# Kernel optimization log

Hardware: AMD Instinct MI355X
Metric: run time of the kernel (lower is better)

## Reference

```python
import jax, jax.numpy as jnp
import numpy as np

ALPHA = 4.0   # spikingjelly surrogate.Sigmoid default
TAU = 2.0
VTH = 1.0
EPS = 1e-5

@jax.custom_vjp
def spike(x):
    return (x >= 0.0).astype(x.dtype)

def _spike_fwd(x):
    return spike(x), x

def _spike_bwd(x, g):
    s = jax.nn.sigmoid(ALPHA * x)
    return (g * ALPHA * s * (1.0 - s),)

spike.defvjp(_spike_fwd, _spike_bwd)

def lif(x):
    # x: [T, B, N, C]; multi-step LIF, v_reset=0 hard reset, detach_reset=True
    def step(v, xt):
        v = v + (xt - v) / TAU          # charge
        s = spike(v - VTH)              # fire (surrogate grad)
        v = v * (1.0 - jax.lax.stop_gradient(s))  # hard reset, detached
        return v, s
    _, out = jax.lax.scan(step, jnp.zeros_like(x[0]), x)
    return out

def bn(x, gamma, beta):
    # BatchNorm1d in training mode: per-channel (last dim) over all other dims
    mu = x.mean(axis=(0, 1, 2), keepdims=True)
    var = x.var(axis=(0, 1, 2), keepdims=True)  # biased var, as torch BN uses for normalization
    return (x - mu) * jax.lax.rsqrt(var + EPS) * gamma + beta

def setup_inputs() -> dict:
    key = jax.random.key(0)
    ks = jax.random.split(key, 3)
    T, B, N, C, H = 4, 32, 1024, 256, 256
    x = jax.random.normal(ks[0], (T, B, N, C), dtype=jnp.float32)
    W1 = jax.random.normal(ks[1], (C, H), dtype=jnp.float32) * (1.0 / np.sqrt(C))
    W2 = jax.random.normal(ks[2], (H, C), dtype=jnp.float32) * (1.0 / np.sqrt(H))
    return {
        "x": x,
        "W1": W1, "b1": jnp.zeros((H,), jnp.float32),
        "gamma1": jnp.ones((H,), jnp.float32), "beta1": jnp.zeros((H,), jnp.float32),
        "W2": W2, "b2": jnp.zeros((C,), jnp.float32),
        "gamma2": jnp.ones((C,), jnp.float32), "beta2": jnp.zeros((C,), jnp.float32),
    }

def reference(x, W1, b1, gamma1, beta1, W2, b2, gamma2, beta2):
    # fc1: Linear -> BN (per-channel over T*B*N) -> multi-step LIF
    h = jnp.einsum('tbnc,ch->tbnh', x, W1) + b1
    h = lif(bn(h, gamma1, beta1))
    # fc2
    o = jnp.einsum('tbnh,ho->tbno', h, W2) + b2
    return lif(bn(o, gamma2, beta2))
```

## Files before the change

kernel.cpp:

```cpp
#include <hip/hip_runtime.h>


typedef __attribute__((ext_vector_type(8))) short bf16x8;
typedef __attribute__((ext_vector_type(8))) _Float16 f16x8;
typedef __attribute__((ext_vector_type(4))) _Float16 f16x4;
typedef __attribute__((ext_vector_type(4))) float f32x4;

__device__ __forceinline__ unsigned short f32_to_bf16_rne(float f) {
    unsigned int u = __builtin_bit_cast(unsigned int, f);
    u += 0x7FFFu + ((u >> 16) & 1u);
    return (unsigned short)(u >> 16);
}
__device__ __forceinline__ float bf16_to_f32(unsigned short h) {
    unsigned int u = ((unsigned int)h) << 16;
    return __builtin_bit_cast(float, u);
}

__global__ __launch_bounds__(256) void split_w1(const float* __restrict__ W1,
                                                _Float16* __restrict__ BhiT,
                                                _Float16* __restrict__ BloT) {
    int i = blockIdx.x * 256 + threadIdx.x;
    int k = i >> 8, n = i & 255;
    float w = W1[i];
    _Float16 hi = (_Float16)w;
    _Float16 lo = (_Float16)((w - (float)hi) * 4096.0f);
    BhiT[(size_t)n * 256 + k] = hi;
    BloT[(size_t)n * 256 + k] = lo;
}

__global__ __launch_bounds__(256) void split_w2(const float* __restrict__ W2,
                                                unsigned short* __restrict__ Bt) {
    int i = blockIdx.x * 256 + threadIdx.x;
    int k = i >> 8, n = i & 255;
    float w = W2[i];
    unsigned short hi = f32_to_bf16_rne(w);
    float r = w - bf16_to_f32(hi);
    unsigned short mid = f32_to_bf16_rne(r);
    float r2 = r - bf16_to_f32(mid);
    unsigned short lo = f32_to_bf16_rne(r2);
    Bt[(size_t)(0 * 256 + n) * 256 + k] = hi;
    Bt[(size_t)(1 * 256 + n) * 256 + k] = mid;
    Bt[(size_t)(2 * 256 + n) * 256 + k] = lo;
}

__global__ __launch_bounds__(512) void gemm1_mfma(const float* __restrict__ A,
                                                  const _Float16* __restrict__ Bhi,
                                                  const _Float16* __restrict__ Blo,
                                                  const float* __restrict__ bias,
                                                  float* __restrict__ C,
                                                  double* __restrict__ partial) {
    __shared__ __align__(16) _Float16 Ahi[128 * 256];
    __shared__ __align__(16) _Float16 Alo[128 * 256];
    const size_t m0 = (size_t)blockIdx.x * 128;
    const int tid = threadIdx.x;
    const int lane = tid & 63;
    const int wave = tid >> 6;
    const int wr = wave >> 2;
    const int wc = wave & 3;
    const int lrow = lane & 15, lchunk = lane >> 4;

    const _Float16* BhiB = Bhi + ((size_t)(64 * wc + lrow)) * 256 + lchunk * 8;
    const _Float16* BloB = Blo + ((size_t)(64 * wc + lrow)) * 256 + lchunk * 8;

    f16x8 bh[2][4], bl[2][4];
#define LOADB1(buf, kk)                                                   \
    _Pragma("unroll") for (int nf = 0; nf < 4; ++nf) {                    \
        bh[buf][nf] = *(const f16x8*)(BhiB + nf * 4096 + (kk) * 32);      \
        bl[buf][nf] = *(const f16x8*)(BloB + nf * 4096 + (kk) * 32);      \
    }

    LOADB1(0, 0)

    {
        const float* src = A + m0 * 256;
#pragma unroll
        for (int it = 0; it < 16; ++it) {
            unsigned i4 = (unsigned)(it * 512 + tid);
            float4 v = *(const float4*)(src + (size_t)i4 * 4);
            float f[4] = {v.x, v.y, v.z, v.w};
            f16x4 hi4, lo4;
#pragma unroll
            for (int e = 0; e < 4; ++e) {
                _Float16 hh = (_Float16)f[e];
                hi4[e] = hh;
                lo4[e] = (_Float16)((f[e] - (float)hh) * 4096.0f);
            }
            unsigned off = i4 * 8u;
            unsigned swz = off ^ (((off >> 9) & 7u) << 4);
            *(f16x4*)((char*)Ahi + swz) = hi4;
            *(f16x4*)((char*)Alo + swz) = lo4;
        }
    }
    __syncthreads();

    f32x4 acc0[4][4] = {}, acc1[4][4] = {};

#pragma unroll
    for (int k0 = 0; k0 < 8; ++k0) {
        const int cur = k0 & 1;
        if (k0 < 7) { LOADB1(cur ^ 1, k0 + 1) }
        f16x8 ah[4], al[4];
#pragma unroll
        for (int mf = 0; mf < 4; ++mf) {
            unsigned r = (unsigned)(64 * wr + 16 * mf + lrow);
            unsigned off = (r * 512u + (unsigned)(k0 * 64 + lchunk * 16)) ^ ((r & 7u) << 4);
            ah[mf] = *(const f16x8*)((const char*)Ahi + off);
            al[mf] = *(const f16x8*)((const char*)Alo + off);
        }
#pragma unroll
        for (int nf = 0; nf < 4; ++nf)
#pragma unroll
            for (int mf = 0; mf < 4; ++mf)
                acc0[mf][nf] = __builtin_amdgcn_mfma_f32_16x16x32_f16(
                    ah[mf], bh[cur][nf], acc0[mf][nf], 0, 0, 0);
#pragma unroll
        for (int nf = 0; nf < 4; ++nf)
#pragma unroll
            for (int mf = 0; mf < 4; ++mf)
                acc1[mf][nf] = __builtin_amdgcn_mfma_f32_16x16x32_f16(
                    ah[mf], bl[cur][nf], acc1[mf][nf], 0, 0, 0);
#pragma unroll
        for (int nf = 0; nf < 4; ++nf)
#pragma unroll
            for (int mf = 0; mf < 4; ++mf)
                acc1[mf][nf] = __builtin_amdgcn_mfma_f32_16x16x32_f16(
                    al[mf], bh[cur][nf], acc1[mf][nf], 0, 0, 0);
    }
#undef LOADB1

    const float UNSCALE = 1.0f / 4096.0f;
    double s[4], q[4];
#pragma unroll
    for (int nf = 0; nf < 4; ++nf) {
        int col = 64 * wc + 16 * nf + lrow;
        float bvv = bias[col];
        double ss = 0.0, qq = 0.0;
#pragma unroll
        for (int mf = 0; mf < 4; ++mf) {
            size_t rowb = m0 + 64 * wr + 16 * mf + 4 * lchunk;
#pragma unroll
            for (int e = 0; e < 4; ++e) {
                float hv = acc0[mf][nf][e] + acc1[mf][nf][e] * UNSCALE + bvv;
                C[(rowb + e) * 256 + col] = hv;
                ss += (double)hv;
                qq += (double)hv * (double)hv;
            }
        }
        s[nf] = ss;
        q[nf] = qq;
    }
#pragma unroll
    for (int nf = 0; nf < 4; ++nf) {
        s[nf] += __shfl_xor(s[nf], 16);
        s[nf] += __shfl_xor(s[nf], 32);
        q[nf] += __shfl_xor(q[nf], 16);
        q[nf] += __shfl_xor(q[nf], 32);
    }
    __syncthreads();
    double* shred = (double*)Ahi;
    if (lane < 16) {
#pragma unroll
        for (int nf = 0; nf < 4; ++nf) {
            shred[(wave * 4 + nf) * 16 + lane] = s[nf];
            shred[512 + (wave * 4 + nf) * 16 + lane] = q[nf];
        }
    }
    __syncthreads();
    if (wave < 4) {
        int nf = lane >> 4, lr = lane & 15;
        int col = 64 * wave + 16 * nf + lr;
        double ssum = shred[(wave * 4 + nf) * 16 + lr] +
                      shred[((4 + wave) * 4 + nf) * 16 + lr];
        double qsum = shred[512 + (wave * 4 + nf) * 16 + lr] +
                      shred[512 + ((4 + wave) * 4 + nf) * 16 + lr];
        partial[(size_t)blockIdx.x * 512 + col] = ssum;
        partial[(size_t)blockIdx.x * 512 + 256 + col] = qsum;
    }
}

__global__ __launch_bounds__(512) void gemm2_fused(const float* __restrict__ h,
                                                   const float2* __restrict__ ss1,
                                                   const unsigned short* __restrict__ Bt,
                                                   const float* __restrict__ bias,
                                                   float* __restrict__ C,
                                                   double* __restrict__ partial,
                                                   int bnRows) {
    __shared__ __align__(16) unsigned short Asw[128 * 256];
    const int bn0 = blockIdx.x * 32;
    const int tid = threadIdx.x;
    const int lane = tid & 63;
    const int wave = tid >> 6;
    const int wr = wave >> 2;
    const int wc = wave & 3;
    const int lrow = lane & 15, lchunk = lane >> 4;

    const unsigned short* Bbase =
        Bt + ((size_t)(64 * wc + lrow)) * 256 + lchunk * 8;

    bf16x8 bb[2][12];
#define LOADB(buf, kk)                                                        \
    _Pragma("unroll") for (int t = 0; t < 3; ++t)                             \
    _Pragma("unroll") for (int nf = 0; nf < 4; ++nf)                          \
        bb[buf][t * 4 + nf] = *(const bf16x8*)(Bbase + (size_t)t * 65536 +    \
                                               nf * 4096 + (kk) * 32);

    LOADB(0, 0)

    {
#pragma unroll
        for (int it = 0; it < 4; ++it) {
            int slot = it * 512 + tid;
            int bn = slot >> 6;
            int colq = slot & 63;
            int c0 = colq * 4;
            float2 p0 = ss1[c0], p1 = ss1[c0 + 1], p2 = ss1[c0 + 2], p3 = ss1[c0 + 3];
            float4 v = make_float4(0.f, 0.f, 0.f, 0.f);
#pragma unroll
            for (int t = 0; t < 4; ++t) {
                float4 hv = *(const float4*)(h + ((size_t)t * bnRows + bn0 + bn) * 256 + c0);
                float x0 = hv.x * p0.x + p0.y;
                float x1 = hv.y * p1.x + p1.y;
                float x2 = hv.z * p2.x + p2.y;
                float x3 = hv.w * p3.x + p3.y;
                v.x = (v.x + x0) * 0.5f;
                v.y = (v.y + x1) * 0.5f;
                v.z = (v.z + x2) * 0.5f;
                v.w = (v.w + x3) * 0.5f;
                ushort4 sp;
                sp.x = (v.x >= 1.0f) ? 0x3F80 : 0;
                sp.y = (v.y >= 1.0f) ? 0x3F80 : 0;
                sp.z = (v.z >= 1.0f) ? 0x3F80 : 0;
                sp.w = (v.w >= 1.0f) ? 0x3F80 : 0;
                v.x = (v.x >= 1.0f) ? 0.0f : v.x;
                v.y = (v.y >= 1.0f) ? 0.0f : v.y;
                v.z = (v.z >= 1.0f) ? 0.0f : v.z;
                v.w = (v.w >= 1.0f) ? 0.0f : v.w;
                unsigned row = (unsigned)(t * 32 + bn);
                unsigned off = (row * 512u + (unsigned)colq * 8u) ^ ((row & 7u) << 4);
                *(ushort4*)((char*)Asw + off) = sp;
            }
        }
    }
    __syncthreads();

    f32x4 acc[4][4] = {};

#pragma unroll
    for (int k0 = 0; k0 < 8; ++k0) {
        const int cur = k0 & 1;
        if (k0 < 7) { LOADB(cur ^ 1, k0 + 1) }
        bf16x8 af[4];
#pragma unroll
        for (int mf = 0; mf < 4; ++mf) {
            unsigned r = (unsigned)(64 * wr + 16 * mf + lrow);
            unsigned off = r * 512u + (unsigned)(k0 * 64 + lchunk * 16);
            off ^= ((r & 7u) << 4);
            af[mf] = *(const bf16x8*)((const char*)Asw + off);
        }
#pragma unroll
        for (int t = 0; t < 3; ++t)
#pragma unroll
            for (int nf = 0; nf < 4; ++nf)
#pragma unroll
                for (int mf = 0; mf < 4; ++mf)
                    acc[mf][nf] = __builtin_amdgcn_mfma_f32_16x16x32_bf16(
                        af[mf], bb[cur][t * 4 + nf], acc[mf][nf], 0, 0, 0);
    }
#undef LOADB

    double s[4], q[4];
#pragma unroll
    for (int nf = 0; nf < 4; ++nf) {
        int col = 64 * wc + 16 * nf + lrow;
        float bvv = bias[col];
        double ss = 0.0, qq = 0.0;
#pragma unroll
        for (int mf = 0; mf < 4; ++mf) {
            int Lbase = 64 * wr + 16 * mf + 4 * lchunk;
#pragma unroll
            for (int e = 0; e < 4; ++e) {
                int L = Lbase + e;
                size_t G = (size_t)(L >> 5) * bnRows + bn0 + (L & 31);
                float hv = acc[mf][nf][e] + bvv;
                C[G * 256 + col] = hv;
                ss += (double)hv;
                qq += (double)hv * (double)hv;
            }
        }
        s[nf] = ss;
        q[nf] = qq;
    }
#pragma unroll
    for (int nf = 0; nf < 4; ++nf) {
        s[nf] += __shfl_xor(s[nf], 16);
        s[nf] += __shfl_xor(s[nf], 32);
        q[nf] += __shfl_xor(q[nf], 16);
        q[nf] += __shfl_xor(q[nf], 32);
    }
    __syncthreads();
    double* shred = (double*)Asw;
    if (lane < 16) {
#pragma unroll
        for (int nf = 0; nf < 4; ++nf) {
            shred[(wave * 4 + nf) * 16 + lane] = s[nf];
            shred[512 + (wave * 4 + nf) * 16 + lane] = q[nf];
        }
    }
    __syncthreads();
    if (wave < 4) {
        int nf = lane >> 4, lr = lane & 15;
        int col = 64 * wave + 16 * nf + lr;
        double ssum = shred[(wave * 4 + nf) * 16 + lr] +
                      shred[((4 + wave) * 4 + nf) * 16 + lr];
        double qsum = shred[512 + (wave * 4 + nf) * 16 + lr] +
                      shred[512 + ((4 + wave) * 4 + nf) * 16 + lr];
        partial[(size_t)blockIdx.x * 512 + col] = ssum;
        partial[(size_t)blockIdx.x * 512 + 256 + col] = qsum;
    }
}

__global__ __launch_bounds__(256) void finalize_stats(const double* __restrict__ partial,
                                                      const float* __restrict__ gamma,
                                                      const float* __restrict__ beta,
                                                      float2* __restrict__ ss,
                                                      int nblocks, double invM) {
    const int c = blockIdx.x;
    const int t = threadIdx.x;
    __shared__ double sh[256];
    __shared__ double sh2[256];
    double s = 0.0, s2 = 0.0;
    for (int b = t; b < nblocks; b += 256) {
        s += partial[(size_t)b * 512 + c];
        s2 += partial[(size_t)b * 512 + 256 + c];
    }
    sh[t] = s;
    sh2[t] = s2;
    __syncthreads();
#pragma unroll
    for (int off = 128; off > 0; off >>= 1) {
        if (t < off) {
            sh[t] += sh[t + off];
            sh2[t] += sh2[t + off];
        }
        __syncthreads();
    }
    if (t == 0) {
        double mu = sh[0] * invM;
        double var = sh2[0] * invM - mu * mu;
        double rstd = 1.0 / sqrt(var + 1e-5);
        double sc = (double)gamma[c] * rstd;
        ss[c] = make_float2((float)sc, (float)((double)beta[c] - mu * sc));
    }
}

__global__ __launch_bounds__(256) void bnlif_f32(const float* __restrict__ h,
                                                 const float2* __restrict__ ss,
                                                 float* __restrict__ out,
                                                 int slab4) {
    int t4 = blockIdx.x * 256 + threadIdx.x;
    if (t4 >= slab4) return;
    size_t idx = (size_t)t4 * 4;
    int c0 = (int)(idx & 255);
    float2 p0 = ss[c0], p1 = ss[c0 + 1], p2 = ss[c0 + 2], p3 = ss[c0 + 3];
    size_t slab = (size_t)slab4 * 4;
    float4 v = make_float4(0.f, 0.f, 0.f, 0.f);
#pragma unroll
    for (int t = 0; t < 4; ++t) {
        float4 hv = *(const float4*)(h + (size_t)t * slab + idx);
        float x0 = hv.x * p0.x + p0.y;
        float x1 = hv.y * p1.x + p1.y;
        float x2 = hv.z * p2.x + p2.y;
        float x3 = hv.w * p3.x + p3.y;
        v.x = (v.x + x0) * 0.5f;
        v.y = (v.y + x1) * 0.5f;
        v.z = (v.z + x2) * 0.5f;
        v.w = (v.w + x3) * 0.5f;
        float4 sp;
        sp.x = (v.x >= 1.0f) ? 1.0f : 0.0f;
        sp.y = (v.y >= 1.0f) ? 1.0f : 0.0f;
        sp.z = (v.z >= 1.0f) ? 1.0f : 0.0f;
        sp.w = (v.w >= 1.0f) ? 1.0f : 0.0f;
        v.x = (v.x >= 1.0f) ? 0.0f : v.x;
        v.y = (v.y >= 1.0f) ? 0.0f : v.y;
        v.z = (v.z >= 1.0f) ? 0.0f : v.z;
        v.w = (v.w >= 1.0f) ? 0.0f : v.w;
        *(float4*)(out + (size_t)t * slab + idx) = sp;
    }
}

extern "C" void kernel_launch(void* const* d_in, const int* in_sizes, int n_in,
                              void* d_out, int out_size, void* d_ws, size_t ws_size,
                              hipStream_t stream) {
    const float* x  = (const float*)d_in[0];
    const float* W1 = (const float*)d_in[1];
    const float* b1 = (const float*)d_in[2];
    const float* g1 = (const float*)d_in[3];
    const float* be1 = (const float*)d_in[4];
    const float* W2 = (const float*)d_in[5];
    const float* b2 = (const float*)d_in[6];
    const float* g2 = (const float*)d_in[7];
    const float* be2 = (const float*)d_in[8];
    float* out = (float*)d_out;

    const int M = in_sizes[0] / 256;
    const int bnRows = M / 4;
    const size_t hBytes = (size_t)M * 256 * 4;

    char* ws = (char*)d_ws;
    float* h = (float*)ws;
    double* partial = (double*)(ws + hBytes);
    unsigned short* W2catT = (unsigned short*)(ws + hBytes + (size_t)1024 * 512 * 8);
    float2* ss1 = (float2*)((char*)W2catT + 3 * 256 * 256 * 2);
    float2* ss2 = ss1 + 256;
    _Float16* W1hiT = (_Float16*)(ss2 + 256);
    _Float16* W1loT = W1hiT + 256 * 256;

    const int slab4 = M * 16;
    const double invM = 1.0 / (double)M;

    dim3 blk(256);

    split_w1<<<dim3(256), blk, 0, stream>>>(W1, W1hiT, W1loT);
    split_w2<<<dim3(256), blk, 0, stream>>>(W2, W2catT);

    gemm1_mfma<<<dim3(M / 128), dim3(512), 0, stream>>>(x, W1hiT, W1loT, b1, h, partial);
    finalize_stats<<<dim3(256), blk, 0, stream>>>(partial, g1, be1, ss1, M / 128, invM);

    gemm2_fused<<<dim3(bnRows / 32), dim3(512), 0, stream>>>(h, ss1, W2catT, b2, h, partial, bnRows);
    finalize_stats<<<dim3(256), blk, 0, stream>>>(partial, g2, be2, ss2, bnRows / 32, invM);
    bnlif_f32<<<dim3(slab4 / 256), blk, 0, stream>>>(h, ss2, out, slab4);
}
```

Baseline: 329.4 us.

## Make GEMM kernels persistent with prefetch of next tile's A slices

Both GEMM kernels now launch a fixed 256-block grid, and each block loops over several 128-row tiles. While the MFMAs for the current tile run, the block loads and converts the next tile's A-operand k-slices into shared memory slice by slice, overlapping global loads with compute. The goal is to cut launch and tail costs and hide A-load latency. In exchange it adds a barrier per k-step and assumes M divides evenly into 256 blocks.

```diff
diff --git a/kernel.cpp b/kernel.cpp
--- a/kernel.cpp
+++ b/kernel.cpp
@@ -48,15 +48,16 @@
                                                   const _Float16* __restrict__ Blo,
                                                   const float* __restrict__ bias,
                                                   float* __restrict__ C,
-                                                  double* __restrict__ partial) {
+                                                  double* __restrict__ partial,
+                                                  int tb) {
     __shared__ __align__(16) _Float16 Ahi[128 * 256];
     __shared__ __align__(16) _Float16 Alo[128 * 256];
-    const size_t m0 = (size_t)blockIdx.x * 128;
+    __shared__ double shred[1056];
+    const size_t mBase = (size_t)blockIdx.x * tb * 128;
     const int tid = threadIdx.x;
     const int lane = tid & 63;
     const int wave = tid >> 6;
-    const int wr = wave >> 2;
-    const int wc = wave & 3;
+    const int wr = wave >> 2, wc = wave & 3;
     const int lrow = lane & 15, lchunk = lane >> 4;
 
     const _Float16* BhiB = Bhi + ((size_t)(64 * wc + lrow)) * 256 + lchunk * 8;
@@ -69,10 +70,8 @@
         bl[buf][nf] = *(const f16x8*)(BloB + nf * 4096 + (kk) * 32);      \
     }
 
-    LOADB1(0, 0)
-
     {
-        const float* src = A + m0 * 256;
+        const float* src = A + mBase * 256;
 #pragma unroll
         for (int it = 0; it < 16; ++it) {
             unsigned i4 = (unsigned)(it * 512 + tid);
@@ -91,91 +90,130 @@
             *(f16x4*)((char*)Alo + swz) = lo4;
         }
     }
-    __syncthreads();
-
-    f32x4 acc0[4][4] = {}, acc1[4][4] = {};
-
-#pragma unroll
-    for (int k0 = 0; k0 < 8; ++k0) {
-        const int cur = k0 & 1;
-        if (k0 < 7) { LOADB1(cur ^ 1, k0 + 1) }
-        f16x8 ah[4], al[4];
-#pragma unroll
-        for (int mf = 0; mf < 4; ++mf) {
-            unsigned r = (unsigned)(64 * wr + 16 * mf + lrow);
-            unsigned off = (r * 512u + (unsigned)(k0 * 64 + lchunk * 16)) ^ ((r & 7u) << 4);
-            ah[mf] = *(const f16x8*)((const char*)Ahi + off);
-            al[mf] = *(const f16x8*)((const char*)Alo + off);
-        }
-#pragma unroll
-        for (int nf = 0; nf < 4; ++nf)
-#pragma unroll
-            for (int mf = 0; mf < 4; ++mf)
-                acc0[mf][nf] = __builtin_amdgcn_mfma_f32_16x16x32_f16(
-                    ah[mf], bh[cur][nf], acc0[mf][nf], 0, 0, 0);
-#pragma unroll
-        for (int nf = 0; nf < 4; ++nf)
-#pragma unroll
-            for (int mf = 0; mf < 4; ++mf)
-                acc1[mf][nf] = __builtin_amdgcn_mfma_f32_16x16x32_f16(
-                    ah[mf], bl[cur][nf], acc1[mf][nf], 0, 0, 0);
-#pragma unroll
-        for (int nf = 0; nf < 4; ++nf)
-#pragma unroll
-            for (int mf = 0; mf < 4; ++mf)
-                acc1[mf][nf] = __builtin_amdgcn_mfma_f32_16x16x32_f16(
-                    al[mf], bh[cur][nf], acc1[mf][nf], 0, 0, 0);
+
+    float4 ldA0, ldA1;
+    const int srow = tid >> 3 << 1;
+#define ISSUE_LDA(tt, kk)                                                       \
+    {                                                                           \
+        const float* s_ = A + (mBase + (size_t)(tt) * 128) * 256;               \
+        unsigned a0 = (unsigned)(0 * 512 + tid);                                \
+        unsigned a1 = (unsigned)(1 * 512 + tid);                                \
+        ldA0 = *(const float4*)(s_ + (size_t)(a0 >> 3) * 256 + (kk) * 32 + (a0 & 7) * 4); \
+        ldA1 = *(const float4*)(s_ + (size_t)(a1 >> 3) * 256 + (kk) * 32 + (a1 & 7) * 4); \
+    }
+#define WRITE_SLICE(kk)                                                         \
+    _Pragma("unroll") for (int it = 0; it < 2; ++it) {                          \
+        unsigned i4s = (unsigned)(it * 512 + tid);                              \
+        unsigned row = i4s >> 3, cq = i4s & 7;                                  \
+        float4 v = it == 0 ? ldA0 : ldA1;                                       \
+        float f[4] = {v.x, v.y, v.z, v.w};                                      \
+        f16x4 hi4, lo4;                                                         \
+        _Pragma("unroll") for (int e = 0; e < 4; ++e) {                         \
+            _Float16 hh = (_Float16)f[e];                                       \
+            hi4[e] = hh;                                                        \
+            lo4[e] = (_Float16)((f[e] - (float)hh) * 4096.0f);                  \
+        }                                                                       \
+        unsigned off = (row * 512u + (kk) * 64u + cq * 8u) ^ ((row & 7u) << 4); \
+        *(f16x4*)((char*)Ahi + off) = hi4;                                      \
+        *(f16x4*)((char*)Alo + off) = lo4;                                      \
+    }
+
+    if (tb > 1) ISSUE_LDA(1, 0)
+
+    for (int t = 0; t < tb; ++t) {
+        LOADB1(0, 0)
+        __syncthreads();
+        f32x4 acc0[4][4] = {}, acc1[4][4] = {};
+#pragma unroll
+        for (int k0 = 0; k0 < 8; ++k0) {
+            const int cur = k0 & 1;
+            if (k0 < 7) { LOADB1(cur ^ 1, k0 + 1) }
+            f16x8 ah[4], al[4];
+#pragma unroll
+            for (int mf = 0; mf < 4; ++mf) {
+                unsigned r = (unsigned)(64 * wr + 16 * mf + lrow);
+                unsigned off = (r * 512u + (unsigned)(k0 * 64 + lchunk * 16)) ^ ((r & 7u) << 4);
+                ah[mf] = *(const f16x8*)((const char*)Ahi + off);
+                al[mf] = *(const f16x8*)((const char*)Alo + off);
+            }
+#pragma unroll
+            for (int nf = 0; nf < 4; ++nf)
+#pragma unroll
+                for (int mf = 0; mf < 4; ++mf)
+                    acc0[mf][nf] = __builtin_amdgcn_mfma_f32_16x16x32_f16(
+                        ah[mf], bh[cur][nf], acc0[mf][nf], 0, 0, 0);
+#pragma unroll
+            for (int nf = 0; nf < 4; ++nf)
+#pragma unroll
+                for (int mf = 0; mf < 4; ++mf)
+                    acc1[mf][nf] = __builtin_amdgcn_mfma_f32_16x16x32_f16(
+                        ah[mf], bl[cur][nf], acc1[mf][nf], 0, 0, 0);
+#pragma unroll
+            for (int nf = 0; nf < 4; ++nf)
+#pragma unroll
+                for (int mf = 0; mf < 4; ++mf)
+                    acc1[mf][nf] = __builtin_amdgcn_mfma_f32_16x16x32_f16(
+                        al[mf], bh[cur][nf], acc1[mf][nf], 0, 0, 0);
+            __syncthreads();
+            if (t < tb - 1) {
+                WRITE_SLICE(k0)
+                if (k0 < 7) { ISSUE_LDA(t + 1, k0 + 1) }
+                else if (t < tb - 2) { ISSUE_LDA(t + 2, 0) }
+            }
+        }
+
+        const size_t m0 = mBase + (size_t)t * 128;
+        const float UNSCALE = 1.0f / 4096.0f;
+        double s[4], q[4];
+#pragma unroll
+        for (int nf = 0; nf < 4; ++nf) {
+            int col = 64 * wc + 16 * nf + lrow;
+            float bvv = bias[col];
+            double ss = 0.0, qq = 0.0;
+#pragma unroll
+            for (int mf = 0; mf < 4; ++mf) {
+                size_t rowb = m0 + 64 * wr + 16 * mf + 4 * lchunk;
+#pragma unroll
+                for (int e = 0; e < 4; ++e) {
+                    float hv = acc0[mf][nf][e] + acc1[mf][nf][e] * UNSCALE + bvv;
+                    C[(rowb + e) * 256 + col] = hv;
+                    ss += (double)hv;
+                    qq += (double)hv * (double)hv;
+                }
+            }
+            s[nf] = ss;
+            q[nf] = qq;
+        }
+#pragma unroll
+        for (int nf = 0; nf < 4; ++nf) {
+            s[nf] += __shfl_xor(s[nf], 16);
+            s[nf] += __shfl_xor(s[nf], 32);
+            q[nf] += __shfl_xor(q[nf], 16);
+            q[nf] += __shfl_xor(q[nf], 32);
+        }
+        if (lane < 16) {
+#pragma unroll
+            for (int nf = 0; nf < 4; ++nf) {
+                shred[(wave * 4 + nf) * 16 + lane] = s[nf];
+                shred[512 + (wave * 4 + nf) * 16 + lane] = q[nf];
+            }
+        }
+        __syncthreads();
+        if (wave < 4) {
+            int nf = lane >> 4, lr = lane & 15;
+            int col = 64 * wave + 16 * nf + lr;
+            double ssum = shred[(wave * 4 + nf) * 16 + lr] +
+                          shred[((4 + wave) * 4 + nf) * 16 + lr];
+            double qsum = shred[512 + (wave * 4 + nf) * 16 + lr] +
+                          shred[512 + ((4 + wave) * 4 + nf) * 16 + lr];
+            partial[((size_t)blockIdx.x * tb + t) * 512 + col] = ssum;
+            partial[((size_t)blockIdx.x * tb + t) * 512 + 256 + col] = qsum;
+        }
+        __syncthreads();
     }
 #undef LOADB1
-
-    const float UNSCALE = 1.0f / 4096.0f;
-    double s[4], q[4];
-#pragma unroll
-    for (int nf = 0; nf < 4; ++nf) {
-        int col = 64 * wc + 16 * nf + lrow;
-        float bvv = bias[col];
-        double ss = 0.0, qq = 0.0;
-#pragma unroll
-        for (int mf = 0; mf < 4; ++mf) {
-            size_t rowb = m0 + 64 * wr + 16 * mf + 4 * lchunk;
-#pragma unroll
-            for (int e = 0; e < 4; ++e) {
-                float hv = acc0[mf][nf][e] + acc1[mf][nf][e] * UNSCALE + bvv;
-                C[(rowb + e) * 256 + col] = hv;
-                ss += (double)hv;
-                qq += (double)hv * (double)hv;
-            }
-        }
-        s[nf] = ss;
-        q[nf] = qq;
-    }
-#pragma unroll
-    for (int nf = 0; nf < 4; ++nf) {
-        s[nf] += __shfl_xor(s[nf], 16);
-        s[nf] += __shfl_xor(s[nf], 32);
-        q[nf] += __shfl_xor(q[nf], 16);
-        q[nf] += __shfl_xor(q[nf], 32);
-    }
-    __syncthreads();
-    double* shred = (double*)Ahi;
-    if (lane < 16) {
-#pragma unroll
-        for (int nf = 0; nf < 4; ++nf) {
-            shred[(wave * 4 + nf) * 16 + lane] = s[nf];
-            shred[512 + (wave * 4 + nf) * 16 + lane] = q[nf];
-        }
-    }
-    __syncthreads();
-    if (wave < 4) {
-        int nf = lane >> 4, lr = lane & 15;
-        int col = 64 * wave + 16 * nf + lr;
-        double ssum = shred[(wave * 4 + nf) * 16 + lr] +
-                      shred[((4 + wave) * 4 + nf) * 16 + lr];
-        double qsum = shred[512 + (wave * 4 + nf) * 16 + lr] +
-                      shred[512 + ((4 + wave) * 4 + nf) * 16 + lr];
-        partial[(size_t)blockIdx.x * 512 + col] = ssum;
-        partial[(size_t)blockIdx.x * 512 + 256 + col] = qsum;
-    }
+#undef ISSUE_LDA
+#undef WRITE_SLICE
 }
 
 __global__ __launch_bounds__(512) void gemm2_fused(const float* __restrict__ h,
@@ -184,14 +222,14 @@
                                                    const float* __restrict__ bias,
                                                    float* __restrict__ C,
                                                    double* __restrict__ partial,
-                                                   int bnRows) {
+                                                   int bnRows, int tb) {
     __shared__ __align__(16) unsigned short Asw[128 * 256];
-    const int bn0 = blockIdx.x * 32;
+    __shared__ double shred[1056];
+    const int bnBase = blockIdx.x * tb * 32;
     const int tid = threadIdx.x;
     const int lane = tid & 63;
     const int wave = tid >> 6;
-    const int wr = wave >> 2;
-    const int wc = wave & 3;
+    const int wr = wave >> 2, wc = wave & 3;
     const int lrow = lane & 15, lchunk = lane >> 4;
 
     const unsigned short* Bbase =
@@ -199,124 +237,143 @@
 
     bf16x8 bb[2][12];
 #define LOADB(buf, kk)                                                        \
-    _Pragma("unroll") for (int t = 0; t < 3; ++t)                             \
+    _Pragma("unroll") for (int t_ = 0; t_ < 3; ++t_)                          \
     _Pragma("unroll") for (int nf = 0; nf < 4; ++nf)                          \
-        bb[buf][t * 4 + nf] = *(const bf16x8*)(Bbase + (size_t)t * 65536 +    \
-                                               nf * 4096 + (kk) * 32);
-
-    LOADB(0, 0)
-
-    {
-#pragma unroll
-        for (int it = 0; it < 4; ++it) {
-            int slot = it * 512 + tid;
-            int bn = slot >> 6;
-            int colq = slot & 63;
-            int c0 = colq * 4;
-            float2 p0 = ss1[c0], p1 = ss1[c0 + 1], p2 = ss1[c0 + 2], p3 = ss1[c0 + 3];
-            float4 v = make_float4(0.f, 0.f, 0.f, 0.f);
-#pragma unroll
-            for (int t = 0; t < 4; ++t) {
-                float4 hv = *(const float4*)(h + ((size_t)t * bnRows + bn0 + bn) * 256 + c0);
-                float x0 = hv.x * p0.x + p0.y;
-                float x1 = hv.y * p1.x + p1.y;
-                float x2 = hv.z * p2.x + p2.y;
-                float x3 = hv.w * p3.x + p3.y;
-                v.x = (v.x + x0) * 0.5f;
-                v.y = (v.y + x1) * 0.5f;
-                v.z = (v.z + x2) * 0.5f;
-                v.w = (v.w + x3) * 0.5f;
-                ushort4 sp;
-                sp.x = (v.x >= 1.0f) ? 0x3F80 : 0;
-                sp.y = (v.y >= 1.0f) ? 0x3F80 : 0;
-                sp.z = (v.z >= 1.0f) ? 0x3F80 : 0;
-                sp.w = (v.w >= 1.0f) ? 0x3F80 : 0;
-                v.x = (v.x >= 1.0f) ? 0.0f : v.x;
-                v.y = (v.y >= 1.0f) ? 0.0f : v.y;
-                v.z = (v.z >= 1.0f) ? 0.0f : v.z;
-                v.w = (v.w >= 1.0f) ? 0.0f : v.w;
-                unsigned row = (unsigned)(t * 32 + bn);
-                unsigned off = (row * 512u + (unsigned)colq * 8u) ^ ((row & 7u) << 4);
-                *(ushort4*)((char*)Asw + off) = sp;
-            }
-        }
-    }
-    __syncthreads();
-
-    f32x4 acc[4][4] = {};
+        bb[buf][t_ * 4 + nf] = *(const bf16x8*)(Bbase + (size_t)t_ * 65536 +  \
+                                                nf * 4096 + (kk) * 32);
+
+    const int sbn = tid >> 3, scq = tid & 7;
+    float4 ldH0, ldH1, ldH2, ldH3, pA, pB;
+#define ISSUE_LDH(tt, kk)                                                            \
+    if (tid < 256) {                                                                 \
+        int c0_ = (kk) * 32 + scq * 4;                                               \
+        size_t rb_ = (size_t)(bnBase + (tt) * 32 + sbn) * 256 + c0_;                 \
+        ldH0 = *(const float4*)(h + 0 * (size_t)bnRows * 256 + rb_);                 \
+        ldH1 = *(const float4*)(h + 1 * (size_t)bnRows * 256 + rb_);                 \
+        ldH2 = *(const float4*)(h + 2 * (size_t)bnRows * 256 + rb_);                 \
+        ldH3 = *(const float4*)(h + 3 * (size_t)bnRows * 256 + rb_);                 \
+        pA = *(const float4*)((const float*)(ss1 + c0_));                            \
+        pB = *(const float4*)((const float*)(ss1 + c0_ + 2));                        \
+    }
+#define WRITE_SLICE2(kk)                                                             \
+    if (tid < 256) {                                                                 \
+        float4 v_ = make_float4(0.f, 0.f, 0.f, 0.f);                                 \
+        _Pragma("unroll") for (int t4 = 0; t4 < 4; ++t4) {                           \
+            float4 hv = t4 == 0 ? ldH0 : t4 == 1 ? ldH1 : t4 == 2 ? ldH2 : ldH3;     \
+            float x0 = hv.x * pA.x + pA.y;                                           \
+            float x1 = hv.y * pA.z + pA.w;                                           \
+            float x2 = hv.z * pB.x + pB.y;                                           \
+            float x3 = hv.w * pB.z + pB.w;                                           \
+            v_.x = (v_.x + x0) * 0.5f;                                               \
+            v_.y = (v_.y + x1) * 0.5f;                                               \
+            v_.z = (v_.z + x2) * 0.5f;                                               \
+            v_.w = (v_.w + x3) * 0.5f;                                               \
+            ushort4 sp;                                                              \
+            sp.x = (v_.x >= 1.0f) ? 0x3F80 : 0;                                      \
+            sp.y = (v_.y >= 1.0f) ? 0x3F80 : 0;                                      \
+            sp.z = (v_.z >= 1.0f) ? 0x3F80 : 0;                                      \
+            sp.w = (v_.w >= 1.0f) ? 0x3F80 : 0;                                      \
+            v_.x = (v_.x >= 1.0f) ? 0.0f : v_.x;                                     \
+            v_.y = (v_.y >= 1.0f) ? 0.0f : v_.y;                                     \
+            v_.z = (v_.z >= 1.0f) ? 0.0f : v_.z;                                     \
+            v_.w = (v_.w >= 1.0f) ? 0.0f : v_.w;                                     \
+            unsigned row = (unsigned)(t4 * 32 + sbn);                                \
+            unsigned off = (row * 512u + (kk) * 64u + scq * 8u) ^ ((row & 7u) << 4); \
+            *(ushort4*)((char*)Asw + off) = sp;                                      \
+        }                                                                            \
+    }
 
 #pragma unroll
     for (int k0 = 0; k0 < 8; ++k0) {
-        const int cur = k0 & 1;
-        if (k0 < 7) { LOADB(cur ^ 1, k0 + 1) }
-        bf16x8 af[4];
-#pragma unroll
-        for (int mf = 0; mf < 4; ++mf) {
-            unsigned r = (unsigned)(64 * wr + 16 * mf + lrow);
-            unsigned off = r * 512u + (unsigned)(k0 * 64 + lchunk * 16);
-            off ^= ((r & 7u) << 4);
-            af[mf] = *(const bf16x8*)((const char*)Asw + off);
-        }
-#pragma unroll
-        for (int t = 0; t < 3; ++t)
-#pragma unroll
-            for (int nf = 0; nf < 4; ++nf)
-#pragma unroll
-                for (int mf = 0; mf < 4; ++mf)
-                    acc[mf][nf] = __builtin_amdgcn_mfma_f32_16x16x32_bf16(
-                        af[mf], bb[cur][t * 4 + nf], acc[mf][nf], 0, 0, 0);
+        ISSUE_LDH(0, k0)
+        WRITE_SLICE2(k0)
+    }
+    if (tb > 1) ISSUE_LDH(1, 0)
+
+    for (int t = 0; t < tb; ++t) {
+        LOADB(0, 0)
+        __syncthreads();
+        f32x4 acc[4][4] = {};
+#pragma unroll
+        for (int k0 = 0; k0 < 8; ++k0) {
+            const int cur = k0 & 1;
+            if (k0 < 7) { LOADB(cur ^ 1, k0 + 1) }
+            bf16x8 af[4];
+#pragma unroll
+            for (int mf = 0; mf < 4; ++mf) {
+                unsigned r = (unsigned)(64 * wr + 16 * mf + lrow);
+                unsigned off = (r * 512u + (unsigned)(k0 * 64 + lchunk * 16)) ^ ((r & 7u) << 4);
+                af[mf] = *(const bf16x8*)((const char*)Asw + off);
+            }
+#pragma unroll
+            for (int t_ = 0; t_ < 3; ++t_)
+#pragma unroll
+                for (int nf = 0; nf < 4; ++nf)
+#pragma unroll
+                    for (int mf = 0; mf < 4; ++mf)
+                        acc[mf][nf] = __builtin_amdgcn_mfma_f32_16x16x32_bf16(
+                            af[mf], bb[cur][t_ * 4 + nf], acc[mf][nf], 0, 0, 0);
+            __syncthreads();
+            if (t < tb - 1) {
+                WRITE_SLICE2(k0)
+                if (k0 < 7) { ISSUE_LDH(t + 1, k0 + 1) }
+                else if (t < tb - 2) { ISSUE_LDH(t + 2, 0) }
+            }
+        }
+
+        const int bn0 = bnBase + t * 32;
+        double s[4], q[4];
+#pragma unroll
+        for (int nf = 0; nf < 4; ++nf) {
+            int col = 64 * wc + 16 * nf + lrow;
+            float bvv = bias[col];
+            double ss = 0.0, qq = 0.0;
+#pragma unroll
+            for (int mf = 0; mf < 4; ++mf) {
+                int Lbase = 64 * wr + 16 * mf + 4 * lchunk;
+#pragma unroll
+                for (int e = 0; e < 4; ++e) {
+                    int L = Lbase + e;
+                    size_t G = (size_t)(L >> 5) * bnRows + bn0 + (L & 31);
+                    float hv = acc[mf][nf][e] + bvv;
+                    C[G * 256 + col] = hv;
+                    ss += (double)hv;
+                    qq += (double)hv * (double)hv;
+                }
+            }
+            s[nf] = ss;
+            q[nf] = qq;
+        }
+#pragma unroll
+        for (int nf = 0; nf < 4; ++nf) {
+            s[nf] += __shfl_xor(s[nf], 16);
+            s[nf] += __shfl_xor(s[nf], 32);
+            q[nf] += __shfl_xor(q[nf], 16);
+            q[nf] += __shfl_xor(q[nf], 32);
+        }
+        if (lane < 16) {
+#pragma unroll
+            for (int nf = 0; nf < 4; ++nf) {
+                shred[(wave * 4 + nf) * 16 + lane] = s[nf];
+                shred[512 + (wave * 4 + nf) * 16 + lane] = q[nf];
+            }
+        }
+        __syncthreads();
+        if (wave < 4) {
+            int nf = lane >> 4, lr = lane & 15;
+            int col = 64 * wave + 16 * nf + lr;
+            double ssum = shred[(wave * 4 + nf) * 16 + lr] +
+                          shred[((4 + wave) * 4 + nf) * 16 + lr];
+            double qsum = shred[512 + (wave * 4 + nf) * 16 + lr] +
+                          shred[512 + ((4 + wave) * 4 + nf) * 16 + lr];
+            partial[((size_t)blockIdx.x * tb + t) * 512 + col] = ssum;
+            partial[((size_t)blockIdx.x * tb + t) * 512 + 256 + col] = qsum;
+        }
+        __syncthreads();
     }
 #undef LOADB
-
-    double s[4], q[4];
-#pragma unroll
-    for (int nf = 0; nf < 4; ++nf) {
-        int col = 64 * wc + 16 * nf + lrow;
-        float bvv = bias[col];
-        double ss = 0.0, qq = 0.0;
-#pragma unroll
-        for (int mf = 0; mf < 4; ++mf) {
-            int Lbase = 64 * wr + 16 * mf + 4 * lchunk;
-#pragma unroll
-            for (int e = 0; e < 4; ++e) {
-                int L = Lbase + e;
-                size_t G = (size_t)(L >> 5) * bnRows + bn0 + (L & 31);
-                float hv = acc[mf][nf][e] + bvv;
-                C[G * 256 + col] = hv;
-                ss += (double)hv;
-                qq += (double)hv * (double)hv;
-            }
-        }
-        s[nf] = ss;
-        q[nf] = qq;
-    }
-#pragma unroll
-    for (int nf = 0; nf < 4; ++nf) {
-        s[nf] += __shfl_xor(s[nf], 16);
-        s[nf] += __shfl_xor(s[nf], 32);
-        q[nf] += __shfl_xor(q[nf], 16);
-        q[nf] += __shfl_xor(q[nf], 32);
-    }
-    __syncthreads();
-    double* shred = (double*)Asw;
-    if (lane < 16) {
-#pragma unroll
-        for (int nf = 0; nf < 4; ++nf) {
-            shred[(wave * 4 + nf) * 16 + lane] = s[nf];
-            shred[512 + (wave * 4 + nf) * 16 + lane] = q[nf];
-        }
-    }
-    __syncthreads();
-    if (wave < 4) {
-        int nf = lane >> 4, lr = lane & 15;
-        int col = 64 * wave + 16 * nf + lr;
-        double ssum = shred[(wave * 4 + nf) * 16 + lr] +
-                      shred[((4 + wave) * 4 + nf) * 16 + lr];
-        double qsum = shred[512 + (wave * 4 + nf) * 16 + lr] +
-                      shred[512 + ((4 + wave) * 4 + nf) * 16 + lr];
-        partial[(size_t)blockIdx.x * 512 + col] = ssum;
-        partial[(size_t)blockIdx.x * 512 + 256 + col] = qsum;
-    }
+#undef ISSUE_LDH
+#undef WRITE_SLICE2
 }
 
 __global__ __launch_bounds__(256) void finalize_stats(const double* __restrict__ partial,
@@ -417,16 +474,18 @@
 
     const int slab4 = M * 16;
     const double invM = 1.0 / (double)M;
+    const int tb1 = (M / 128) / 256;
+    const int tb2 = (bnRows / 32) / 256;
 
     dim3 blk(256);
 
     split_w1<<<dim3(256), blk, 0, stream>>>(W1, W1hiT, W1loT);
     split_w2<<<dim3(256), blk, 0, stream>>>(W2, W2catT);
 
-    gemm1_mfma<<<dim3(M / 128), dim3(512), 0, stream>>>(x, W1hiT, W1loT, b1, h, partial);
-    finalize_stats<<<dim3(256), blk, 0, stream>>>(partial, g1, be1, ss1, M / 128, invM);
-
-    gemm2_fused<<<dim3(bnRows / 32), dim3(512), 0, stream>>>(h, ss1, W2catT, b2, h, partial, bnRows);
-    finalize_stats<<<dim3(256), blk, 0, stream>>>(partial, g2, be2, ss2, bnRows / 32, invM);
+    gemm1_mfma<<<dim3(256), dim3(512), 0, stream>>>(x, W1hiT, W1loT, b1, h, partial, tb1);
+    finalize_stats<<<dim3(256), blk, 0, stream>>>(partial, g1, be1, ss1, 256 * tb1, invM);
+
+    gemm2_fused<<<dim3(256), dim3(512), 0, stream>>>(h, ss1, W2catT, b2, h, partial, bnRows, tb2);
+    finalize_stats<<<dim3(256), blk, 0, stream>>>(partial, g2, be2, ss2, 256 * tb2, invM);
     bnlif_f32<<<dim3(slab4 / 256), blk, 0, stream>>>(h, ss2, out, slab4);
 }
```

New measurement: 583.6 us. 1.77x slower.

## Halve GEMM block tiles to 64 rows with 4 waves for two blocks per CU

Applied to the files above, without the earlier changes.

Both GEMM kernels move from 128-row tiles and 8 waves per block to 64-row tiles and 4 waves, with launch bounds requesting two resident blocks per CU. This halves LDS per block and doubles the grid (M/64 blocks), so more blocks can overlap their load and compute phases. With one wave per column slice, the cross-wave LDS reduction of BN statistics is dropped and each wave writes its per-column partials directly. The cost is twice as many partial rows for finalize_stats to sum, a larger partial buffer in the workspace, and B-weight fragments re-read from global memory by twice as many blocks.

```diff
diff --git a/kernel.cpp b/kernel.cpp
--- a/kernel.cpp
+++ b/kernel.cpp
@@ -43,20 +43,18 @@
     Bt[(size_t)(2 * 256 + n) * 256 + k] = lo;
 }
 
-__global__ __launch_bounds__(512) void gemm1_mfma(const float* __restrict__ A,
-                                                  const _Float16* __restrict__ Bhi,
-                                                  const _Float16* __restrict__ Blo,
-                                                  const float* __restrict__ bias,
-                                                  float* __restrict__ C,
-                                                  double* __restrict__ partial) {
-    __shared__ __align__(16) _Float16 Ahi[128 * 256];
-    __shared__ __align__(16) _Float16 Alo[128 * 256];
-    const size_t m0 = (size_t)blockIdx.x * 128;
+__global__ __launch_bounds__(256, 2) void gemm1_mfma(const float* __restrict__ A,
+                                                     const _Float16* __restrict__ Bhi,
+                                                     const _Float16* __restrict__ Blo,
+                                                     const float* __restrict__ bias,
+                                                     float* __restrict__ C,
+                                                     double* __restrict__ partial) {
+    __shared__ __align__(16) _Float16 Ahi[64 * 256];
+    __shared__ __align__(16) _Float16 Alo[64 * 256];
+    const size_t m0 = (size_t)blockIdx.x * 64;
     const int tid = threadIdx.x;
     const int lane = tid & 63;
-    const int wave = tid >> 6;
-    const int wr = wave >> 2;
-    const int wc = wave & 3;
+    const int wc = tid >> 6;
     const int lrow = lane & 15, lchunk = lane >> 4;
 
     const _Float16* BhiB = Bhi + ((size_t)(64 * wc + lrow)) * 256 + lchunk * 8;
@@ -75,7 +73,7 @@
         const float* src = A + m0 * 256;
 #pragma unroll
         for (int it = 0; it < 16; ++it) {
-            unsigned i4 = (unsigned)(it * 512 + tid);
+            unsigned i4 = (unsigned)(it * 256 + tid);
             float4 v = *(const float4*)(src + (size_t)i4 * 4);
             float f[4] = {v.x, v.y, v.z, v.w};
             f16x4 hi4, lo4;
@@ -102,7 +100,7 @@
         f16x8 ah[4], al[4];
 #pragma unroll
         for (int mf = 0; mf < 4; ++mf) {
-            unsigned r = (unsigned)(64 * wr + 16 * mf + lrow);
+            unsigned r = (unsigned)(16 * mf + lrow);
             unsigned off = (r * 512u + (unsigned)(k0 * 64 + lchunk * 16)) ^ ((r & 7u) << 4);
             ah[mf] = *(const f16x8*)((const char*)Ahi + off);
             al[mf] = *(const f16x8*)((const char*)Alo + off);
@@ -129,7 +127,6 @@
 #undef LOADB1
 
     const float UNSCALE = 1.0f / 4096.0f;
-    double s[4], q[4];
 #pragma unroll
     for (int nf = 0; nf < 4; ++nf) {
         int col = 64 * wc + 16 * nf + lrow;
@@ -137,7 +134,7 @@
         double ss = 0.0, qq = 0.0;
 #pragma unroll
         for (int mf = 0; mf < 4; ++mf) {
-            size_t rowb = m0 + 64 * wr + 16 * mf + 4 * lchunk;
+            size_t rowb = m0 + 16 * mf + 4 * lchunk;
 #pragma unroll
             for (int e = 0; e < 4; ++e) {
                 float hv = acc0[mf][nf][e] + acc1[mf][nf][e] * UNSCALE + bvv;
@@ -146,52 +143,29 @@
                 qq += (double)hv * (double)hv;
             }
         }
-        s[nf] = ss;
-        q[nf] = qq;
-    }
-#pragma unroll
-    for (int nf = 0; nf < 4; ++nf) {
-        s[nf] += __shfl_xor(s[nf], 16);
-        s[nf] += __shfl_xor(s[nf], 32);
-        q[nf] += __shfl_xor(q[nf], 16);
-        q[nf] += __shfl_xor(q[nf], 32);
-    }
-    __syncthreads();
-    double* shred = (double*)Ahi;
-    if (lane < 16) {
-#pragma unroll
-        for (int nf = 0; nf < 4; ++nf) {
-            shred[(wave * 4 + nf) * 16 + lane] = s[nf];
-            shred[512 + (wave * 4 + nf) * 16 + lane] = q[nf];
-        }
-    }
-    __syncthreads();
-    if (wave < 4) {
-        int nf = lane >> 4, lr = lane & 15;
-        int col = 64 * wave + 16 * nf + lr;
-        double ssum = shred[(wave * 4 + nf) * 16 + lr] +
-                      shred[((4 + wave) * 4 + nf) * 16 + lr];
-        double qsum = shred[512 + (wave * 4 + nf) * 16 + lr] +
-                      shred[512 + ((4 + wave) * 4 + nf) * 16 + lr];
-        partial[(size_t)blockIdx.x * 512 + col] = ssum;
-        partial[(size_t)blockIdx.x * 512 + 256 + col] = qsum;
-    }
-}
-
-__global__ __launch_bounds__(512) void gemm2_fused(const float* __restrict__ h,
-                                                   const float2* __restrict__ ss1,
-                                                   const unsigned short* __restrict__ Bt,
-                                                   const float* __restrict__ bias,
-                                                   float* __restrict__ C,
-                                                   double* __restrict__ partial,
-                                                   int bnRows) {
-    __shared__ __align__(16) unsigned short Asw[128 * 256];
-    const int bn0 = blockIdx.x * 32;
+        ss += __shfl_xor(ss, 16);
+        ss += __shfl_xor(ss, 32);
+        qq += __shfl_xor(qq, 16);
+        qq += __shfl_xor(qq, 32);
+        if (lane < 16) {
+            partial[(size_t)blockIdx.x * 512 + col] = ss;
+            partial[(size_t)blockIdx.x * 512 + 256 + col] = qq;
+        }
+    }
+}
+
+__global__ __launch_bounds__(256, 2) void gemm2_fused(const float* __restrict__ h,
+                                                      const float2* __restrict__ ss1,
+                                                      const unsigned short* __restrict__ Bt,
+                                                      const float* __restrict__ bias,
+                                                      float* __restrict__ C,
+                                                      double* __restrict__ partial,
+                                                      int bnRows) {
+    __shared__ __align__(16) unsigned short Asw[64 * 256];
+    const int bn0 = blockIdx.x * 16;
     const int tid = threadIdx.x;
     const int lane = tid & 63;
-    const int wave = tid >> 6;
-    const int wr = wave >> 2;
-    const int wc = wave & 3;
+    const int wc = tid >> 6;
     const int lrow = lane & 15, lchunk = lane >> 4;
 
     const unsigned short* Bbase =
@@ -199,25 +173,26 @@
 
     bf16x8 bb[2][12];
 #define LOADB(buf, kk)                                                        \
-    _Pragma("unroll") for (int t = 0; t < 3; ++t)                             \
+    _Pragma("unroll") for (int t_ = 0; t_ < 3; ++t_)                          \
     _Pragma("unroll") for (int nf = 0; nf < 4; ++nf)                          \
-        bb[buf][t * 4 + nf] = *(const bf16x8*)(Bbase + (size_t)t * 65536 +    \
-                                               nf * 4096 + (kk) * 32);
+        bb[buf][t_ * 4 + nf] = *(const bf16x8*)(Bbase + (size_t)t_ * 65536 +  \
+                                                nf * 4096 + (kk) * 32);
 
     LOADB(0, 0)
 
     {
 #pragma unroll
         for (int it = 0; it < 4; ++it) {
-            int slot = it * 512 + tid;
+            int slot = it * 256 + tid;
             int bn = slot >> 6;
             int colq = slot & 63;
             int c0 = colq * 4;
             float2 p0 = ss1[c0], p1 = ss1[c0 + 1], p2 = ss1[c0 + 2], p3 = ss1[c0 + 3];
+            size_t rb = (size_t)(bn0 + bn) * 256 + c0;
             float4 v = make_float4(0.f, 0.f, 0.f, 0.f);
 #pragma unroll
-            for (int t = 0; t < 4; ++t) {
-                float4 hv = *(const float4*)(h + ((size_t)t * bnRows + bn0 + bn) * 256 + c0);
+            for (int t4 = 0; t4 < 4; ++t4) {
+                float4 hv = *(const float4*)(h + (size_t)t4 * bnRows * 256 + rb);
                 float x0 = hv.x * p0.x + p0.y;
                 float x1 = hv.y * p1.x + p1.y;
                 float x2 = hv.z * p2.x + p2.y;
@@ -235,7 +210,7 @@
                 v.y = (v.y >= 1.0f) ? 0.0f : v.y;
                 v.z = (v.z >= 1.0f) ? 0.0f : v.z;
                 v.w = (v.w >= 1.0f) ? 0.0f : v.w;
-                unsigned row = (unsigned)(t * 32 + bn);
+                unsigned row = (unsigned)(t4 * 16 + bn);
                 unsigned off = (row * 512u + (unsigned)colq * 8u) ^ ((row & 7u) << 4);
                 *(ushort4*)((char*)Asw + off) = sp;
             }
@@ -252,23 +227,21 @@
         bf16x8 af[4];
 #pragma unroll
         for (int mf = 0; mf < 4; ++mf) {
-            unsigned r = (unsigned)(64 * wr + 16 * mf + lrow);
-            unsigned off = r * 512u + (unsigned)(k0 * 64 + lchunk * 16);
-            off ^= ((r & 7u) << 4);
+            unsigned r = (unsigned)(16 * mf + lrow);
+            unsigned off = (r * 512u + (unsigned)(k0 * 64 + lchunk * 16)) ^ ((r & 7u) << 4);
             af[mf] = *(const bf16x8*)((const char*)Asw + off);
         }
 #pragma unroll
-        for (int t = 0; t < 3; ++t)
+        for (int t_ = 0; t_ < 3; ++t_)
 #pragma unroll
             for (int nf = 0; nf < 4; ++nf)
 #pragma unroll
                 for (int mf = 0; mf < 4; ++mf)
                     acc[mf][nf] = __builtin_amdgcn_mfma_f32_16x16x32_bf16(
-                        af[mf], bb[cur][t * 4 + nf], acc[mf][nf], 0, 0, 0);
+                        af[mf], bb[cur][t_ * 4 + nf], acc[mf][nf], 0, 0, 0);
     }
 #undef LOADB
 
-    double s[4], q[4];
 #pragma unroll
     for (int nf = 0; nf < 4; ++nf) {
         int col = 64 * wc + 16 * nf + lrow;
@@ -276,46 +249,25 @@
         double ss = 0.0, qq = 0.0;
 #pragma unroll
         for (int mf = 0; mf < 4; ++mf) {
-            int Lbase = 64 * wr + 16 * mf + 4 * lchunk;
+            int Lbase = 16 * mf + 4 * lchunk;
 #pragma unroll
             for (int e = 0; e < 4; ++e) {
                 int L = Lbase + e;
-                size_t G = (size_t)(L >> 5) * bnRows + bn0 + (L & 31);
+                size_t G = (size_t)(L >> 4) * bnRows + bn0 + (L & 15);
                 float hv = acc[mf][nf][e] + bvv;
                 C[G * 256 + col] = hv;
                 ss += (double)hv;
                 qq += (double)hv * (double)hv;
             }
         }
-        s[nf] = ss;
-        q[nf] = qq;
-    }
-#pragma unroll
-    for (int nf = 0; nf < 4; ++nf) {
-        s[nf] += __shfl_xor(s[nf], 16);
-        s[nf] += __shfl_xor(s[nf], 32);
-        q[nf] += __shfl_xor(q[nf], 16);
-        q[nf] += __shfl_xor(q[nf], 32);
-    }
-    __syncthreads();
-    double* shred = (double*)Asw;
-    if (lane < 16) {
-#pragma unroll
-        for (int nf = 0; nf < 4; ++nf) {
-            shred[(wave * 4 + nf) * 16 + lane] = s[nf];
-            shred[512 + (wave * 4 + nf) * 16 + lane] = q[nf];
-        }
-    }
-    __syncthreads();
-    if (wave < 4) {
-        int nf = lane >> 4, lr = lane & 15;
-        int col = 64 * wave + 16 * nf + lr;
-        double ssum = shred[(wave * 4 + nf) * 16 + lr] +
-                      shred[((4 + wave) * 4 + nf) * 16 + lr];
-        double qsum = shred[512 + (wave * 4 + nf) * 16 + lr] +
-                      shred[512 + ((4 + wave) * 4 + nf) * 16 + lr];
-        partial[(size_t)blockIdx.x * 512 + col] = ssum;
-        partial[(size_t)blockIdx.x * 512 + 256 + col] = qsum;
+        ss += __shfl_xor(ss, 16);
+        ss += __shfl_xor(ss, 32);
+        qq += __shfl_xor(qq, 16);
+        qq += __shfl_xor(qq, 32);
+        if (lane < 16) {
+            partial[(size_t)blockIdx.x * 512 + col] = ss;
+            partial[(size_t)blockIdx.x * 512 + 256 + col] = qq;
+        }
     }
 }
 
@@ -409,7 +361,7 @@
     char* ws = (char*)d_ws;
     float* h = (float*)ws;
     double* partial = (double*)(ws + hBytes);
-    unsigned short* W2catT = (unsigned short*)(ws + hBytes + (size_t)1024 * 512 * 8);
+    unsigned short* W2catT = (unsigned short*)(ws + hBytes + (size_t)2048 * 512 * 8);
     float2* ss1 = (float2*)((char*)W2catT + 3 * 256 * 256 * 2);
     float2* ss2 = ss1 + 256;
     _Float16* W1hiT = (_Float16*)(ss2 + 256);
@@ -417,16 +369,18 @@
 
     const int slab4 = M * 16;
     const double invM = 1.0 / (double)M;
+    const int NB1 = M / 64;
+    const int NB2 = bnRows / 16;
 
     dim3 blk(256);
 
     split_w1<<<dim3(256), blk, 0, stream>>>(W1, W1hiT, W1loT);
     split_w2<<<dim3(256), blk, 0, stream>>>(W2, W2catT);
 
-    gemm1_mfma<<<dim3(M / 128), dim3(512), 0, stream>>>(x, W1hiT, W1loT, b1, h, partial);
-    finalize_stats<<<dim3(256), blk, 0, stream>>>(partial, g1, be1, ss1, M / 128, invM);
-
-    gemm2_fused<<<dim3(bnRows / 32), dim3(512), 0, stream>>>(h, ss1, W2catT, b2, h, partial, bnRows);
-    finalize_stats<<<dim3(256), blk, 0, stream>>>(partial, g2, be2, ss2, bnRows / 32, invM);
+    gemm1_mfma<<<dim3(NB1), blk, 0, stream>>>(x, W1hiT, W1loT, b1, h, partial);
+    finalize_stats<<<dim3(256), blk, 0, stream>>>(partial, g1, be1, ss1, NB1, invM);
+
+    gemm2_fused<<<dim3(NB2), blk, 0, stream>>>(h, ss1, W2catT, b2, h, partial, bnRows);
+    finalize_stats<<<dim3(256), blk, 0, stream>>>(partial, g2, be2, ss2, NB2, invM);
     bnlif_f32<<<dim3(slab4 / 256), blk, 0, stream>>>(h, ss2, out, slab4);
 }
```

Measured after the change: 303.8 us. -7.8%, faster.
